# Kernel optimization log

Measured on AMD Instinct MI355X. Metric: run time of the kernel, lower is better.

The kernel has to match this reference:

```python
import jax, jax.numpy as jnp
import numpy as np

B, N, H = 8, 2048, 256


def setup_inputs() -> dict:
    key = jax.random.key(0)
    ks = jax.random.split(key, 8)
    s = 1.0 / np.sqrt(H)
    return {
        "node": jax.random.normal(ks[0], (B, N, H), dtype=jnp.float32),
        "graph": jax.random.uniform(ks[1], (B, N, N), dtype=jnp.float32),
        "W1": jax.random.normal(ks[2], (H, H), dtype=jnp.float32) * s,
        "b1": jnp.zeros((H,), dtype=jnp.float32),
        "W2": jax.random.normal(ks[3], (H, H), dtype=jnp.float32) * s,
        "b2": jnp.zeros((H,), dtype=jnp.float32),
        "Wout": jax.random.normal(ks[4], (H, 2 * H), dtype=jnp.float32) * (1.0 / np.sqrt(2 * H)),
        "bout": jnp.zeros((H,), dtype=jnp.float32),
    }


def reference(node, graph, W1, b1, W2, b2, Wout, bout):
    # Symmetric normalization D^{-1/2} A D^{-1/2}, batched and vectorized
    # (equivalent to the per-sample diag-mm loop in the original).
    d = jnp.sum(graph, axis=2)                # [B, N] row sums (torch sum(1) on [N,N])
    dinv = d ** -0.5                          # [B, N]
    g = graph * dinv[:, :, None] * dinv[:, None, :]  # [B, N, N]

    # node_info = relu(fc1(g @ node)); fc2(g @ node_info)
    h = jax.nn.relu(jnp.einsum("bnm,bmh->bnh", g, node) @ W1.T + b1)
    h = jax.nn.relu(jnp.einsum("bnm,bmh->bnh", g, h) @ W2.T + b2)

    agg = jnp.concatenate([node, h], axis=2)  # [B, N, 2H]
    return jax.nn.relu(agg @ Wout.T + bout)   # [B, N, H]
```

## Files before the change

kernel.cpp:

```cpp
#include <hip/hip_runtime.h>
#include <stdint.h>

typedef __attribute__((ext_vector_type(4))) float f32x4;
typedef __attribute__((ext_vector_type(8))) short bf16x8;

static __device__ __forceinline__ unsigned short f2bf(float x) {
  unsigned int u = __builtin_bit_cast(unsigned int, x);
  u = (u + 0x7fffu + ((u >> 16) & 1u)) >> 16;
  return (unsigned short)u;
}

#define GLD16(g, l)                                                            \
  __builtin_amdgcn_global_load_lds(                                            \
      (__attribute__((address_space(1))) const void*)(g),                      \
      (__attribute__((address_space(3))) void*)(l), 16, 0, 0)

__global__ __launch_bounds__(256) void rowscale_cvt_k(
    const float* __restrict__ g, float* __restrict__ dinv,
    unsigned short* __restrict__ gb) {
  int row = blockIdx.x * 4 + (threadIdx.x >> 6);
  int lane = threadIdx.x & 63;
  const float* p = g + (long)row * 2048;
  float4 v[8];
  float s = 0.f;
#pragma unroll
  for (int i = 0; i < 8; ++i) {
    v[i] = *(const float4*)(p + (lane + i * 64) * 4);
    s += v[i].x + v[i].y + v[i].z + v[i].w;
  }
#pragma unroll
  for (int off = 32; off; off >>= 1) s += __shfl_xor(s, off, 64);
  float di = rsqrtf(s);
  if (lane == 0) dinv[row] = di;
  unsigned short* q = gb + (long)row * 2048;
#pragma unroll
  for (int i = 0; i < 8; ++i) {
    ushort4 u;
    u.x = f2bf(v[i].x * di); u.y = f2bf(v[i].y * di);
    u.z = f2bf(v[i].z * di); u.w = f2bf(v[i].w * di);
    *(ushort4*)(q + (lane + i * 64) * 4) = u;
  }
}

__global__ __launch_bounds__(256) void cvt_w_k(const float* __restrict__ W1,
                                               const float* __restrict__ W2,
                                               const float* __restrict__ Wout,
                                               unsigned short* __restrict__ wb) {
  int idx = blockIdx.x * 256 + threadIdx.x;
  float v;
  if (idx < 65536) v = W1[idx];
  else if (idx < 131072) v = W2[idx - 65536];
  else v = Wout[idx - 131072];
  wb[idx] = f2bf(v);
}

__global__ __launch_bounds__(256) void prep_node_k(
    const float* __restrict__ node, const float* __restrict__ dinv,
    unsigned short* __restrict__ nodeT, unsigned short* __restrict__ agg) {
  __shared__ unsigned short t[64 * 68];
  int tid = threadIdx.x;
  int m0 = blockIdx.x * 64, h0 = blockIdx.y * 64;
  long b = blockIdx.z;
#pragma unroll
  for (int i = 0; i < 4; ++i) {
    int idx = tid + 256 * i;
    int r = idx >> 4, c4 = idx & 15;
    long m = m0 + r;
    float4 v = *(const float4*)(node + (b * 2048 + m) * 256 + h0 + c4 * 4);
    float di = dinv[b * 2048 + m];
    ushort4 u;
    u.x = f2bf(v.x); u.y = f2bf(v.y); u.z = f2bf(v.z); u.w = f2bf(v.w);
    *(ushort4*)(agg + (b * 2048 + m) * 512 + h0 + c4 * 4) = u;
    t[(c4 * 4 + 0) * 68 + r] = f2bf(v.x * di);
    t[(c4 * 4 + 1) * 68 + r] = f2bf(v.y * di);
    t[(c4 * 4 + 2) * 68 + r] = f2bf(v.z * di);
    t[(c4 * 4 + 3) * 68 + r] = f2bf(v.w * di);
  }
  __syncthreads();
#pragma unroll
  for (int i = 0; i < 4; ++i) {
    int idx = tid + 256 * i;
    int hr = idx >> 4, c4 = idx & 15;
    ushort4 o = *(const ushort4*)(&t[hr * 68 + c4 * 4]);
    *(ushort4*)(nodeT + (b * 256 + h0 + hr) * 2048 + m0 + c4 * 4) = o;
  }
}

template <bool BIAS, bool RELU, bool SCALE, bool TRANS, bool OUTF32>
__global__ __launch_bounds__(512, 1) void gemm128(
    const unsigned short* __restrict__ A, const unsigned short* __restrict__ Bt,
    const float* __restrict__ bias, const float* __restrict__ scale,
    void* __restrict__ Cp, int K, int lda, int ldbt, long bBatch, int ldc) {
  __shared__ char lds[98304];
  char* ldsA = lds;
  char* ldsB = lds + 32768;

  int tid = threadIdx.x;
  int lane = tid & 63;
  int w = tid >> 6;
  int wm = w >> 2, wn = w & 3;

  int bid = blockIdx.x;
  int tile = ((bid & 7) << 4) + (bid >> 3);
  long row0 = (long)tile * 128;
  int batch = (int)(row0 >> 11);
  const unsigned short* Bb = Bt + (long)batch * bBatch;

  int nt = K >> 6;
  f32x4 acc[4][4] = {};

  auto stageA = [&](int kt, int buf) {
#pragma unroll
    for (int i = 0; i < 2; ++i) {
      int slot = i * 512 + tid;
      int r = slot >> 3, j = slot & 7;
      int jg = j ^ (r & 7);
      GLD16(A + (row0 + r) * lda + kt * 64 + jg * 8,
            ldsA + buf * 16384 + (i * 8 + w) * 1024);
    }
  };
  auto stageB = [&](int kt, int buf) {
#pragma unroll
    for (int i = 0; i < 4; ++i) {
      int slot = i * 512 + tid;
      int c = slot >> 3, j = slot & 7;
      int jg = j ^ (c & 7);
      GLD16(Bb + (long)c * ldbt + kt * 64 + jg * 8,
            ldsB + buf * 32768 + (i * 8 + w) * 1024);
    }
  };
  auto compute = [&](int buf) {
    char* bA = ldsA + buf * 16384;
    char* bB = ldsB + buf * 32768;
    bf16x8 a[4][2], bb[4][2];
#pragma unroll
    for (int m = 0; m < 4; ++m)
#pragma unroll
      for (int kk = 0; kk < 2; ++kk) {
        int row = wm * 64 + m * 16 + (lane & 15);
        int off = (row * 128 + kk * 64 + (lane >> 4) * 16) ^ ((row & 7) << 4);
        a[m][kk] = *(const bf16x8*)(bA + off);
      }
#pragma unroll
    for (int n = 0; n < 4; ++n)
#pragma unroll
      for (int kk = 0; kk < 2; ++kk) {
        int col = wn * 64 + n * 16 + (lane & 15);
        int off = (col * 128 + kk * 64 + (lane >> 4) * 16) ^ ((col & 7) << 4);
        bb[n][kk] = *(const bf16x8*)(bB + off);
      }
#pragma unroll
    for (int m = 0; m < 4; ++m)
#pragma unroll
      for (int n = 0; n < 4; ++n) {
        acc[m][n] = __builtin_amdgcn_mfma_f32_16x16x32_bf16(a[m][0], bb[n][0],
                                                            acc[m][n], 0, 0, 0);
        acc[m][n] = __builtin_amdgcn_mfma_f32_16x16x32_bf16(a[m][1], bb[n][1],
                                                            acc[m][n], 0, 0, 0);
      }
  };

  stageA(0, 0);
  stageB(0, 0);
  __syncthreads();

  int cur = 0;
  for (int t = 0; t < nt; ++t) {
    int nxt = cur ^ 1;
    if (t + 1 < nt) {
      stageA(t + 1, nxt);
      stageB(t + 1, nxt);
    }
    compute(cur);
    __syncthreads();
    cur = nxt;
  }

  if (TRANS) {
    unsigned short* tb = (unsigned short*)lds;
#pragma unroll
    for (int m = 0; m < 4; ++m)
#pragma unroll
      for (int n = 0; n < 4; ++n) {
        int col = wn * 64 + n * 16 + (lane & 15);
        float bv = BIAS ? bias[col] : 0.f;
#pragma unroll
        for (int r = 0; r < 4; ++r) {
          int rl = wm * 64 + m * 16 + (lane >> 4) * 4 + r;
          float v = acc[m][n][r];
          if (BIAS) v += bv;
          if (RELU) v = fmaxf(v, 0.f);
          if (SCALE) v *= scale[row0 + rl];
          tb[col * 136 + rl] = f2bf(v);
        }
      }
    __syncthreads();
    unsigned short* C = (unsigned short*)Cp;
    int rin = (int)(row0 & 2047);
#pragma unroll
    for (int i = 0; i < 8; ++i) {
      int id = i * 512 + tid;
      int col = id >> 4, seg = id & 15;
      bf16x8 u = *(const bf16x8*)(tb + col * 136 + seg * 8);
      *(bf16x8*)(C + ((long)batch * 256 + col) * 2048 + rin + seg * 8) = u;
    }
  } else {
#pragma unroll
    for (int m = 0; m < 4; ++m)
#pragma unroll
      for (int n = 0; n < 4; ++n) {
        int col = wn * 64 + n * 16 + (lane & 15);
        float bv = BIAS ? bias[col] : 0.f;
#pragma unroll
        for (int r = 0; r < 4; ++r) {
          long row = row0 + wm * 64 + m * 16 + (lane >> 4) * 4 + r;
          float v = acc[m][n][r];
          if (BIAS) v += bv;
          if (RELU) v = fmaxf(v, 0.f);
          if (SCALE) v *= scale[row];
          if (OUTF32) ((float*)Cp)[row * ldc + col] = v;
          else ((unsigned short*)Cp)[row * ldc + col] = f2bf(v);
        }
      }
  }
}

extern "C" void kernel_launch(void* const* d_in, const int* in_sizes, int n_in,
                              void* d_out, int out_size, void* d_ws,
                              size_t ws_size, hipStream_t stream) {
  const float* node = (const float*)d_in[0];
  const float* graph = (const float*)d_in[1];
  const float* W1 = (const float*)d_in[2];
  const float* b1 = (const float*)d_in[3];
  const float* W2 = (const float*)d_in[4];
  const float* b2 = (const float*)d_in[5];
  const float* Wout = (const float*)d_in[6];
  const float* bout = (const float*)d_in[7];
  float* out = (float*)d_out;

  char* p = (char*)d_ws;
  float* dinv = (float*)p;                    p += 16384 * 4;
  unsigned short* wb = (unsigned short*)p;    p += 262144 * 2;
  unsigned short* gb = (unsigned short*)p;    p += 8L * 2048 * 2048 * 2;
  unsigned short* nodeT = (unsigned short*)p; p += 8L * 256 * 2048 * 2;
  unsigned short* bufT = (unsigned short*)p;  p += 8L * 2048 * 256 * 2;
  unsigned short* agg = (unsigned short*)p;   p += 8L * 2048 * 512 * 2;

  rowscale_cvt_k<<<4096, 256, 0, stream>>>(graph, dinv, gb);
  cvt_w_k<<<1024, 256, 0, stream>>>(W1, W2, Wout, wb);
  prep_node_k<<<dim3(32, 4, 8), 256, 0, stream>>>(node, dinv, nodeT, agg);

  gemm128<false, false, false, false, false><<<128, 512, 0, stream>>>(
      gb, nodeT, nullptr, nullptr, bufT, 2048, 2048, 2048, 256L * 2048, 256);
  gemm128<true, true, true, true, false><<<128, 512, 0, stream>>>(
      bufT, wb, b1, dinv, nodeT, 256, 256, 256, 0, 2048);
  gemm128<false, false, false, false, false><<<128, 512, 0, stream>>>(
      gb, nodeT, nullptr, nullptr, bufT, 2048, 2048, 2048, 256L * 2048, 256);
  gemm128<true, true, false, false, false><<<128, 512, 0, stream>>>(
      bufT, wb + 65536, b2, nullptr, agg + 256, 256, 256, 256, 0, 512);
  gemm128<true, true, false, false, true><<<128, 512, 0, stream>>>(
      agg, wb + 131072, bout, nullptr, out, 512, 512, 512, 0, 256);
}
```

Measured before the change: 320.3 us.

## Split GEMM tiles into 128x128 blocks to double grid size

Changes the GEMM from 128x256 output tiles with 512 threads to 128x128 tiles with 256 threads, launching 256 blocks instead of 128. On a 256-CU MI355X the previous grid left half the CUs idle. The new grid fills all CUs, and launch bounds allow two blocks per CU with less LDS each. The cost is that each A tile is now loaded twice, once per column half, and each block does less MFMA work per byte loaded.

New measurement: 310.0 us. -3.2%, faster.

```diff
diff --git a/kernel.cpp b/kernel.cpp
--- a/kernel.cpp
+++ b/kernel.cpp
@@ -87,23 +87,25 @@
 }
 
 template <bool BIAS, bool RELU, bool SCALE, bool TRANS, bool OUTF32>
-__global__ __launch_bounds__(512, 1) void gemm128(
+__global__ __launch_bounds__(256, 2) void gemm_t(
     const unsigned short* __restrict__ A, const unsigned short* __restrict__ Bt,
     const float* __restrict__ bias, const float* __restrict__ scale,
     void* __restrict__ Cp, int K, int lda, int ldbt, long bBatch, int ldc) {
-  __shared__ char lds[98304];
+  __shared__ char lds[65536];
   char* ldsA = lds;
   char* ldsB = lds + 32768;
 
   int tid = threadIdx.x;
   int lane = tid & 63;
   int w = tid >> 6;
-  int wm = w >> 2, wn = w & 3;
+  int wm = w >> 1, wn = w & 1;
 
   int bid = blockIdx.x;
-  int tile = ((bid & 7) << 4) + (bid >> 3);
-  long row0 = (long)tile * 128;
-  int batch = (int)(row0 >> 11);
+  int gt = ((bid & 7) << 5) + (bid >> 3);
+  int mt = gt >> 1;
+  int col0 = (gt & 1) * 128;
+  long row0 = (long)mt * 128;
+  int batch = mt >> 4;
   const unsigned short* Bb = Bt + (long)batch * bBatch;
 
   int nt = K >> 6;
@@ -111,27 +113,27 @@
 
   auto stageA = [&](int kt, int buf) {
 #pragma unroll
-    for (int i = 0; i < 2; ++i) {
-      int slot = i * 512 + tid;
+    for (int i = 0; i < 4; ++i) {
+      int slot = i * 256 + tid;
       int r = slot >> 3, j = slot & 7;
       int jg = j ^ (r & 7);
-      GLD16(A + (row0 + r) * lda + kt * 64 + jg * 8,
-            ldsA + buf * 16384 + (i * 8 + w) * 1024);
+      GLD16(A + (row0 + r) * (long)lda + kt * 64 + jg * 8,
+            ldsA + buf * 16384 + (i * 4 + w) * 1024);
     }
   };
   auto stageB = [&](int kt, int buf) {
 #pragma unroll
     for (int i = 0; i < 4; ++i) {
-      int slot = i * 512 + tid;
+      int slot = i * 256 + tid;
       int c = slot >> 3, j = slot & 7;
       int jg = j ^ (c & 7);
-      GLD16(Bb + (long)c * ldbt + kt * 64 + jg * 8,
-            ldsB + buf * 32768 + (i * 8 + w) * 1024);
+      GLD16(Bb + (long)(col0 + c) * ldbt + kt * 64 + jg * 8,
+            ldsB + buf * 16384 + (i * 4 + w) * 1024);
     }
   };
   auto compute = [&](int buf) {
     char* bA = ldsA + buf * 16384;
-    char* bB = ldsB + buf * 32768;
+    char* bB = ldsB + buf * 16384;
     bf16x8 a[4][2], bb[4][2];
 #pragma unroll
     for (int m = 0; m < 4; ++m)
@@ -182,8 +184,8 @@
     for (int m = 0; m < 4; ++m)
 #pragma unroll
       for (int n = 0; n < 4; ++n) {
-        int col = wn * 64 + n * 16 + (lane & 15);
-        float bv = BIAS ? bias[col] : 0.f;
+        int lc = wn * 64 + n * 16 + (lane & 15);
+        float bv = BIAS ? bias[col0 + lc] : 0.f;
 #pragma unroll
         for (int r = 0; r < 4; ++r) {
           int rl = wm * 64 + m * 16 + (lane >> 4) * 4 + r;
@@ -191,7 +193,7 @@
           if (BIAS) v += bv;
           if (RELU) v = fmaxf(v, 0.f);
           if (SCALE) v *= scale[row0 + rl];
-          tb[col * 136 + rl] = f2bf(v);
+          tb[lc * 136 + rl] = f2bf(v);
         }
       }
     __syncthreads();
@@ -199,17 +201,17 @@
     int rin = (int)(row0 & 2047);
 #pragma unroll
     for (int i = 0; i < 8; ++i) {
-      int id = i * 512 + tid;
-      int col = id >> 4, seg = id & 15;
-      bf16x8 u = *(const bf16x8*)(tb + col * 136 + seg * 8);
-      *(bf16x8*)(C + ((long)batch * 256 + col) * 2048 + rin + seg * 8) = u;
+      int id = i * 256 + tid;
+      int lc = id >> 4, seg = id & 15;
+      bf16x8 u = *(const bf16x8*)(tb + lc * 136 + seg * 8);
+      *(bf16x8*)(C + ((long)batch * 256 + col0 + lc) * 2048 + rin + seg * 8) = u;
     }
   } else {
 #pragma unroll
     for (int m = 0; m < 4; ++m)
 #pragma unroll
       for (int n = 0; n < 4; ++n) {
-        int col = wn * 64 + n * 16 + (lane & 15);
+        int col = col0 + wn * 64 + n * 16 + (lane & 15);
         float bv = BIAS ? bias[col] : 0.f;
 #pragma unroll
         for (int r = 0; r < 4; ++r) {
@@ -250,14 +252,14 @@
   cvt_w_k<<<1024, 256, 0, stream>>>(W1, W2, Wout, wb);
   prep_node_k<<<dim3(32, 4, 8), 256, 0, stream>>>(node, dinv, nodeT, agg);
 
-  gemm128<false, false, false, false, false><<<128, 512, 0, stream>>>(
+  gemm_t<false, false, false, false, false><<<256, 256, 0, stream>>>(
       gb, nodeT, nullptr, nullptr, bufT, 2048, 2048, 2048, 256L * 2048, 256);
-  gemm128<true, true, true, true, false><<<128, 512, 0, stream>>>(
+  gemm_t<true, true, true, true, false><<<256, 256, 0, stream>>>(
       bufT, wb, b1, dinv, nodeT, 256, 256, 256, 0, 2048);
-  gemm128<false, false, false, false, false><<<128, 512, 0, stream>>>(
+  gemm_t<false, false, false, false, false><<<256, 256, 0, stream>>>(
       gb, nodeT, nullptr, nullptr, bufT, 2048, 2048, 2048, 256L * 2048, 256);
-  gemm128<true, true, false, false, false><<<128, 512, 0, stream>>>(
+  gemm_t<true, true, false, false, false><<<256, 256, 0, stream>>>(
       bufT, wb + 65536, b2, nullptr, agg + 256, 256, 256, 256, 0, 512);
-  gemm128<true, true, false, false, true><<<128, 512, 0, stream>>>(
+  gemm_t<true, true, false, false, true><<<256, 256, 0, stream>>>(
       agg, wb + 131072, bout, nullptr, out, 512, 512, 512, 0, 256);
 }
```
